# Kernel tuning notes

Measured on AMD Instinct MI355X. Metric: run time of the kernel, lower is better.

The kernel has to match this reference:

```python
import jax, jax.numpy as jnp
import numpy as np

B, T, F_, H1, H2, HEADS = 64, 128, 64, 32, 64, 4
E = H2 * F_  # embed_dim = hidden_dims[-1] * feats = 4096


def conv2d(x, w, b):
    # x: [b,c,H,W], w: [o,c,kh,kw], SAME padding (kernel 3 -> pad 1)
    y = jax.lax.conv_general_dilated(x, w, (1, 1), 'SAME',
                                     dimension_numbers=('NCHW', 'OIHW', 'NCHW'))
    return y + b[None, :, None, None]


def gru_layer(xs, h0, wg, bg, wc, bc):
    # xs: [b,t,c,H,W]; h0: [b,h,H,W]. Standard ConvGRU cell:
    #   r,u = sigmoid(conv([x,h])); cand = tanh(conv([x, r*h]))
    #   h' = (1-u)*h + u*cand
    def step(h, x):
        g = conv2d(jnp.concatenate([x, h], axis=1), wg, bg)
        r, u = jnp.split(jax.nn.sigmoid(g), 2, axis=1)
        cand = jnp.tanh(conv2d(jnp.concatenate([x, r * h], axis=1), wc, bc))
        h_next = (1.0 - u) * h + u * cand
        return h_next, h_next
    hT, ys = jax.lax.scan(step, h0, jnp.swapaxes(xs, 0, 1))
    return jnp.swapaxes(ys, 0, 1), hT  # [b,t,h,H,W], [b,h,H,W]


def mha(q, k, v, w_qkv, b_qkv, w_out, b_out):
    # q: [b,1,E], k/v: [b,t,E]; torch nn.MultiheadAttention (eval, no dropout)
    wq, wk, wv = jnp.split(w_qkv, 3, axis=0)
    bq, bk, bv = jnp.split(b_qkv, 3, axis=0)
    dh = E // HEADS
    def heads(x, w, bb):
        y = x @ w.T + bb
        b_, l_, _ = y.shape
        return y.reshape(b_, l_, HEADS, dh).transpose(0, 2, 1, 3)  # [b,h,l,dh]
    qh, kh, vh = heads(q, wq, bq), heads(k, wk, bk), heads(v, wv, bv)
    scores = jnp.einsum('bhqd,bhkd->bhqk', qh, kh) / jnp.sqrt(jnp.float32(dh))
    attn = jax.nn.softmax(scores, axis=-1)
    ctx = jnp.einsum('bhqk,bhkd->bhqd', attn, vh)
    ctx = ctx.transpose(0, 2, 1, 3).reshape(q.shape[0], q.shape[1], E)
    return ctx @ w_out.T + b_out


def setup_inputs() -> dict:
    key = jax.random.key(0)
    ks = jax.random.split(key, 24)
    s = 0.05
    d = {'x': jax.random.normal(ks[0], (B, T, F_), dtype=jnp.float32)}
    # encoder layer 0: in=1, h=H1; layer 1: in=H1, h=H2
    d['wg_e0'] = jax.random.normal(ks[1], (2 * H1, 1 + H1, 3, 3)) * s
    d['bg_e0'] = jnp.zeros((2 * H1,))
    d['wc_e0'] = jax.random.normal(ks[2], (H1, 1 + H1, 3, 3)) * s
    d['bc_e0'] = jnp.zeros((H1,))
    d['wg_e1'] = jax.random.normal(ks[3], (2 * H2, H1 + H2, 3, 3)) * s
    d['bg_e1'] = jnp.zeros((2 * H2,))
    d['wc_e1'] = jax.random.normal(ks[4], (H2, H1 + H2, 3, 3)) * s
    d['bc_e1'] = jnp.zeros((H2,))
    # decoder: input dim = 2*H2; hidden dims reversed [H2, H1]
    d['wg_d0'] = jax.random.normal(ks[5], (2 * H2, 2 * H2 + H2, 3, 3)) * s
    d['bg_d0'] = jnp.zeros((2 * H2,))
    d['wc_d0'] = jax.random.normal(ks[6], (H2, 2 * H2 + H2, 3, 3)) * s
    d['bc_d0'] = jnp.zeros((H2,))
    d['wg_d1'] = jax.random.normal(ks[7], (2 * H1, H2 + H1, 3, 3)) * s
    d['bg_d1'] = jnp.zeros((2 * H1,))
    d['wc_d1'] = jax.random.normal(ks[8], (H1, H2 + H1, 3, 3)) * s
    d['bc_d1'] = jnp.zeros((H1,))
    d['w_qkv'] = jax.random.normal(ks[9], (3 * E, E)) * (1.0 / np.sqrt(E))
    d['b_qkv'] = jnp.zeros((3 * E,))
    d['w_out'] = jax.random.normal(ks[10], (E, E)) * (1.0 / np.sqrt(E))
    d['b_out'] = jnp.zeros((E,))
    d['w_fin'] = jax.random.normal(ks[11], (1, H1, 1, 1)) * s
    d['b_fin'] = jnp.zeros((1,))
    return d


def reference(x, wg_e0, bg_e0, wc_e0, bc_e0, wg_e1, bg_e1, wc_e1, bc_e1,
              wg_d0, bg_d0, wc_d0, bc_d0, wg_d1, bg_d1, wc_d1, bc_d1,
              w_qkv, b_qkv, w_out, b_out, w_fin, b_fin):
    b, t, f = x.shape
    xr = x.reshape(b, t, 1, f, 1)
    # encoder (2 ConvGRU layers, zero init states)
    y0, h0 = gru_layer(xr, jnp.zeros((b, H1, f, 1), x.dtype), wg_e0, bg_e0, wc_e0, bc_e0)
    y1, h1 = gru_layer(y0, jnp.zeros((b, H2, f, 1), x.dtype), wg_e1, bg_e1, wc_e1, bc_e1)
    # attention bottleneck: query = last hidden, memory = encoder outputs
    query = h1.reshape(b, 1, E)
    memory = y1.reshape(b, t, E)
    context = mha(query, memory, memory, w_qkv, b_qkv, w_out, b_out)  # [b,1,E]
    ctx = context.reshape(b, 1, H2, f, 1)
    dec_in = jnp.concatenate([y1, jnp.broadcast_to(ctx, (b, t, H2, f, 1))], axis=2)
    # decoder init states: encoder last states reversed -> [h1 (H2), h0 (H1)]
    z0, _ = gru_layer(dec_in, h1, wg_d0, bg_d0, wc_d0, bc_d0)
    z1, _ = gru_layer(z0, h0, wg_d1, bg_d1, wc_d1, bc_d1)  # [b,t,H1,f,1]
    # final 1x1 conv applied per timestep == channel contraction
    rec = jnp.einsum('btcfw,oc->btofw', z1, w_fin[:, :, 0, 0]) + b_fin[None, None, :, None, None]
    return rec.reshape(b, t, f)
```

## Files before the change

kernel.cpp:

```cpp
#include <hip/hip_runtime.h>
#include <cstdint>


#define B_  64
#define T_  128
#define TC  16
#define NCH 8

__device__ __forceinline__ float wsum(float v) {
#pragma unroll
  for (int m = 32; m > 0; m >>= 1) v += __shfl_xor(v, m, 64);
  return v;
}
__device__ __forceinline__ float wmaxr(float v) {
#pragma unroll
  for (int m = 32; m > 0; m >>= 1) v = fmaxf(v, __shfl_xor(v, m, 64));
  return v;
}
__device__ __forceinline__ float sigmoidf_(float x) {
  return 1.f / (1.f + __expf(-x));
}
__device__ __forceinline__ float tanhf_(float x) {
  x = fminf(fmaxf(x, -15.f), 15.f);
  float e2 = __expf(2.f * x);
  return (e2 - 1.f) / (e2 + 1.f);
}

struct PackArgs {
  const float* src[16];
  float* dst[16];
  int intot[16];
  int ic0[16];
  int icn[16];
  int oc[16];
};

__global__ __launch_bounds__(256) void pack_all_kernel(PackArgs pa) {
  const int j = blockIdx.y;
  const int icN = pa.icn[j];
  const int total = pa.oc[j] * icN * 3;
  const int i = blockIdx.x * 256 + threadIdx.x;
  if (i >= total) return;
  const int per_oc = icN * 3;
  const int oc = i / per_oc;
  const int rem = i - oc * per_oc;
  const int ic = rem / 3, dk = rem - ic * 3;
  pa.dst[j][i] =
      pa.src[j][((size_t)(oc * pa.intot[j] + pa.ic0[j] + ic) * 3 + dk) * 3 + 1];
}

template <int INC, int OG, int OCC>
__device__ __forceinline__ void conv_x_body(
    float (*sin_)[72], int tid, int b, int tl, int oidx,
    const float* __restrict__ seq, int seqC, size_t sB,
    const float* __restrict__ ctx,
    const float* __restrict__ Wgx, const float* __restrict__ Wcx,
    const float* __restrict__ bg, const float* __restrict__ bc,
    float* __restrict__ out) {
  constexpr int OCT = OG + OCC;
  constexpr int NJ = OG / 32;
  constexpr int NJC = OCC / 32;
  const int ocg = tid >> 3;
  const int f0 = (tid & 7) << 3;

  for (int idx = tid; idx < INC * 72; idx += 256) {
    int ic = idx / 72, ff = idx - ic * 72;
    float v = 0.f;
    if (ff >= 1 && ff <= 64) {
      int fs = ff - 1;
      v = (ic < seqC)
              ? seq[(size_t)b * sB + (size_t)tl * seqC * 64 + ic * 64 + fs]
              : ctx[((size_t)b * (INC - seqC) + (ic - seqC)) * 64 + fs];
    }
    sin_[ic][ff] = v;
  }
  __syncthreads();

  if constexpr (INC >= 4) {
    {
      float acc[NJ][8];
#pragma unroll
      for (int j = 0; j < NJ; ++j) {
        float bb = bg[ocg + 32 * j];
#pragma unroll
        for (int ff = 0; ff < 8; ++ff) acc[j][ff] = bb;
      }
      for (int ic0 = 0; ic0 < INC; ic0 += 4) {
        float hv[4][10];
#pragma unroll
        for (int q = 0; q < 4; ++q) {
          float4 a4 = *(const float4*)&sin_[ic0 + q][f0];
          float4 b4 = *(const float4*)&sin_[ic0 + q][f0 + 4];
          float2 c2 = *(const float2*)&sin_[ic0 + q][f0 + 8];
          hv[q][0] = a4.x; hv[q][1] = a4.y; hv[q][2] = a4.z; hv[q][3] = a4.w;
          hv[q][4] = b4.x; hv[q][5] = b4.y; hv[q][6] = b4.z; hv[q][7] = b4.w;
          hv[q][8] = c2.x; hv[q][9] = c2.y;
        }
#pragma unroll
        for (int j = 0; j < NJ; ++j) {
          const int oc = ocg + 32 * j;
          const float4* w4 = (const float4*)(Wgx + ((size_t)oc * INC + ic0) * 3);
          float4 wa = w4[0], wb = w4[1], wc4 = w4[2];
          const float wt[12] = {wa.x, wa.y, wa.z, wa.w, wb.x, wb.y, wb.z, wb.w,
                                wc4.x, wc4.y, wc4.z, wc4.w};
#pragma unroll
          for (int q = 0; q < 4; ++q) {
            const float w0 = wt[3 * q], w1 = wt[3 * q + 1], w2 = wt[3 * q + 2];
#pragma unroll
            for (int ff = 0; ff < 8; ++ff)
              acc[j][ff] = fmaf(w0, hv[q][ff], fmaf(w1, hv[q][ff + 1], fmaf(w2, hv[q][ff + 2], acc[j][ff])));
          }
        }
      }
#pragma unroll
      for (int j = 0; j < NJ; ++j) {
        float* dst = out + ((size_t)oidx * OCT + ocg + 32 * j) * 64 + f0;
        *(float4*)dst = make_float4(acc[j][0], acc[j][1], acc[j][2], acc[j][3]);
        *(float4*)(dst + 4) = make_float4(acc[j][4], acc[j][5], acc[j][6], acc[j][7]);
      }
    }
    {
      float acc[NJC][8];
#pragma unroll
      for (int j = 0; j < NJC; ++j) {
        float bb = bc[ocg + 32 * j];
#pragma unroll
        for (int ff = 0; ff < 8; ++ff) acc[j][ff] = bb;
      }
      for (int ic0 = 0; ic0 < INC; ic0 += 4) {
        float hv[4][10];
#pragma unroll
        for (int q = 0; q < 4; ++q) {
          float4 a4 = *(const float4*)&sin_[ic0 + q][f0];
          float4 b4 = *(const float4*)&sin_[ic0 + q][f0 + 4];
          float2 c2 = *(const float2*)&sin_[ic0 + q][f0 + 8];
          hv[q][0] = a4.x; hv[q][1] = a4.y; hv[q][2] = a4.z; hv[q][3] = a4.w;
          hv[q][4] = b4.x; hv[q][5] = b4.y; hv[q][6] = b4.z; hv[q][7] = b4.w;
          hv[q][8] = c2.x; hv[q][9] = c2.y;
        }
#pragma unroll
        for (int j = 0; j < NJC; ++j) {
          const int oc = ocg + 32 * j;
          const float4* w4 = (const float4*)(Wcx + ((size_t)oc * INC + ic0) * 3);
          float4 wa = w4[0], wb = w4[1], wc4 = w4[2];
          const float wt[12] = {wa.x, wa.y, wa.z, wa.w, wb.x, wb.y, wb.z, wb.w,
                                wc4.x, wc4.y, wc4.z, wc4.w};
#pragma unroll
          for (int q = 0; q < 4; ++q) {
            const float w0 = wt[3 * q], w1 = wt[3 * q + 1], w2 = wt[3 * q + 2];
#pragma unroll
            for (int ff = 0; ff < 8; ++ff)
              acc[j][ff] = fmaf(w0, hv[q][ff], fmaf(w1, hv[q][ff + 1], fmaf(w2, hv[q][ff + 2], acc[j][ff])));
          }
        }
      }
#pragma unroll
      for (int j = 0; j < NJC; ++j) {
        float* dst = out + ((size_t)oidx * OCT + OG + ocg + 32 * j) * 64 + f0;
        *(float4*)dst = make_float4(acc[j][0], acc[j][1], acc[j][2], acc[j][3]);
        *(float4*)(dst + 4) = make_float4(acc[j][4], acc[j][5], acc[j][6], acc[j][7]);
      }
    }
  } else {
    float hv[10];
    {
      float4 a4 = *(const float4*)&sin_[0][f0];
      float4 b4 = *(const float4*)&sin_[0][f0 + 4];
      float2 c2 = *(const float2*)&sin_[0][f0 + 8];
      hv[0] = a4.x; hv[1] = a4.y; hv[2] = a4.z; hv[3] = a4.w;
      hv[4] = b4.x; hv[5] = b4.y; hv[6] = b4.z; hv[7] = b4.w;
      hv[8] = c2.x; hv[9] = c2.y;
    }
#pragma unroll
    for (int j = 0; j < NJ; ++j) {
      const int oc = ocg + 32 * j;
      const float w0 = Wgx[oc * 3], w1 = Wgx[oc * 3 + 1], w2 = Wgx[oc * 3 + 2];
      float acc[8];
#pragma unroll
      for (int ff = 0; ff < 8; ++ff)
        acc[ff] = fmaf(w0, hv[ff], fmaf(w1, hv[ff + 1], fmaf(w2, hv[ff + 2], bg[oc])));
      float* dst = out + ((size_t)oidx * OCT + oc) * 64 + f0;
      *(float4*)dst = make_float4(acc[0], acc[1], acc[2], acc[3]);
      *(float4*)(dst + 4) = make_float4(acc[4], acc[5], acc[6], acc[7]);
    }
#pragma unroll
    for (int j = 0; j < NJC; ++j) {
      const int oc = ocg + 32 * j;
      const float w0 = Wcx[oc * 3], w1 = Wcx[oc * 3 + 1], w2 = Wcx[oc * 3 + 2];
      float acc[8];
#pragma unroll
      for (int ff = 0; ff < 8; ++ff)
        acc[ff] = fmaf(w0, hv[ff], fmaf(w1, hv[ff + 1], fmaf(w2, hv[ff + 2], bc[oc])));
      float* dst = out + ((size_t)oidx * OCT + OG + oc) * 64 + f0;
      *(float4*)dst = make_float4(acc[0], acc[1], acc[2], acc[3]);
      *(float4*)(dst + 4) = make_float4(acc[4], acc[5], acc[6], acc[7]);
    }
  }
}

template <int INC, int OG, int OCC>
__global__ __launch_bounds__(256) void conv_x_kernel(
    const float* __restrict__ seq, int seqC, size_t sB,
    const float* __restrict__ ctx,
    const float* __restrict__ Wgx, const float* __restrict__ Wcx,
    const float* __restrict__ bg, const float* __restrict__ bc,
    float* __restrict__ out, int tdiv) {
  __shared__ float sin_[INC][72];
  const int b = blockIdx.x / tdiv;
  const int tl = blockIdx.x - b * tdiv;
  conv_x_body<INC, OG, OCC>(sin_, threadIdx.x, b, tl, blockIdx.x, seq, seqC,
                            sB, ctx, Wgx, Wcx, bg, bc, out);
}

__device__ __forceinline__ void final_body(
    int tid, int tile, const float* __restrict__ z1c,
    const float* __restrict__ wfin, const float* __restrict__ bfin,
    float* __restrict__ out, int tOff) {
  const int idx = tile * 256 + tid;
  const int f = idx & 63;
  const int tl = (idx >> 6) & (TC - 1);
  const int b = idx >> 10;
  const float* zp = z1c + ((size_t)b * TC + tl) * 2048 + f;
  float a = bfin[0];
#pragma unroll
  for (int c = 0; c < 32; ++c) a = fmaf(wfin[c], zp[c * 64], a);
  out[(size_t)b * 8192 + (size_t)(tOff + tl) * 64 + f] = a;
}

__global__ __launch_bounds__(256) void final_kernel(
    const float* __restrict__ z1c,
    const float* __restrict__ wfin, const float* __restrict__ bfin,
    float* __restrict__ out, int tOff) {
  final_body(threadIdx.x, blockIdx.x, z1c, wfin, bfin, out, tOff);
}

template <int HC>
__device__ __forceinline__ void gru_body(
    float* smem,
    const float* __restrict__ A, size_t aB,
    const float* __restrict__ Wgh, const float* __restrict__ Wch,
    const float* hinit,
    float* __restrict__ Y, size_t yB, float* hfinal, int b) {
  constexpr int NR = HC / 32;
  constexpr int OG = 2 * HC;
  constexpr int OCT = 3 * HC;
  float(*Hs)[68] = (float(*)[68])smem;
  float(*Rs)[68] = (float(*)[68])(smem + HC * 68);
  const int tid = threadIdx.x;
  const int ocg = tid >> 4;
  const int f0 = (tid & 15) << 2;
  const int im = (f0 == 0) ? 0 : f0 - 1;
  const bool lo = (f0 == 0), hi = (f0 == 60);

  float hreg[NR][4];
#pragma unroll
  for (int r = 0; r < NR; ++r) {
    const int oc = ocg + 32 * r;
    const float4 v = *(const float4*)(hinit + ((size_t)b * HC + oc) * 64 + f0);
    hreg[r][0] = v.x; hreg[r][1] = v.y; hreg[r][2] = v.z; hreg[r][3] = v.w;
    *(float4*)&Hs[oc][f0] = v;
  }
  __syncthreads();
  __builtin_amdgcn_s_setprio(1);

  for (int tl = 0; tl < TC; ++tl) {
    const float* Abt = A + (size_t)b * aB + (size_t)tl * (OCT * 64);
    float accr[NR][4], accu[NR][4], accc[NR][4];
#pragma unroll
    for (int r = 0; r < NR; ++r) {
      const int oc = ocg + 32 * r;
      const float4 vr = *(const float4*)(Abt + (size_t)oc * 64 + f0);
      const float4 vu = *(const float4*)(Abt + (size_t)(HC + oc) * 64 + f0);
      const float4 vc = *(const float4*)(Abt + (size_t)(OG + oc) * 64 + f0);
      accr[r][0] = vr.x; accr[r][1] = vr.y; accr[r][2] = vr.z; accr[r][3] = vr.w;
      accu[r][0] = vu.x; accu[r][1] = vu.y; accu[r][2] = vu.z; accu[r][3] = vu.w;
      accc[r][0] = vc.x; accc[r][1] = vc.y; accc[r][2] = vc.z; accc[r][3] = vc.w;
    }
#pragma unroll 2
    for (int hc0 = 0; hc0 < HC; hc0 += 4) {
      float hv[4][6];
#pragma unroll
      for (int q = 0; q < 4; ++q) {
        const float4 h4 = *(const float4*)&Hs[hc0 + q][f0];
        const float lf = Hs[hc0 + q][im];
        const float rt = Hs[hc0 + q][f0 + 4];
        hv[q][0] = lo ? 0.f : lf;
        hv[q][1] = h4.x; hv[q][2] = h4.y; hv[q][3] = h4.z; hv[q][4] = h4.w;
        hv[q][5] = hi ? 0.f : rt;
      }
#pragma unroll
      for (int r = 0; r < NR; ++r) {
        {
          const float4* w4 = (const float4*)(Wgh + ((size_t)(ocg + 32 * r) * HC + hc0) * 3);
          const float4 wa = w4[0], wb = w4[1], wc4 = w4[2];
          const float wt[12] = {wa.x, wa.y, wa.z, wa.w, wb.x, wb.y, wb.z, wb.w,
                                wc4.x, wc4.y, wc4.z, wc4.w};
#pragma unroll
          for (int q = 0; q < 4; ++q) {
            const float w0 = wt[3 * q], w1 = wt[3 * q + 1], w2 = wt[3 * q + 2];
#pragma unroll
            for (int ff = 0; ff < 4; ++ff)
              accr[r][ff] = fmaf(w0, hv[q][ff], fmaf(w1, hv[q][ff + 1], fmaf(w2, hv[q][ff + 2], accr[r][ff])));
          }
        }
        {
          const float4* w4 = (const float4*)(Wgh + ((size_t)(HC + ocg + 32 * r) * HC + hc0) * 3);
          const float4 wa = w4[0], wb = w4[1], wc4 = w4[2];
          const float wt[12] = {wa.x, wa.y, wa.z, wa.w, wb.x, wb.y, wb.z, wb.w,
                                wc4.x, wc4.y, wc4.z, wc4.w};
#pragma unroll
          for (int q = 0; q < 4; ++q) {
            const float w0 = wt[3 * q], w1 = wt[3 * q + 1], w2 = wt[3 * q + 2];
#pragma unroll
            for (int ff = 0; ff < 4; ++ff)
              accu[r][ff] = fmaf(w0, hv[q][ff], fmaf(w1, hv[q][ff + 1], fmaf(w2, hv[q][ff + 2], accu[r][ff])));
          }
        }
      }
    }
    float uu[NR][4];
#pragma unroll
    for (int r = 0; r < NR; ++r) {
      float4 rh;
#pragma unroll
      for (int ff = 0; ff < 4; ++ff) {
        uu[r][ff] = sigmoidf_(accu[r][ff]);
        (&rh.x)[ff] = sigmoidf_(accr[r][ff]) * hreg[r][ff];
      }
      *(float4*)&Rs[ocg + 32 * r][f0] = rh;
    }
    __syncthreads();
#pragma unroll 2
    for (int hc0 = 0; hc0 < HC; hc0 += 4) {
      float hv[4][6];
#pragma unroll
      for (int q = 0; q < 4; ++q) {
        const float4 h4 = *(const float4*)&Rs[hc0 + q][f0];
        const float lf = Rs[hc0 + q][im];
        const float rt = Rs[hc0 + q][f0 + 4];
        hv[q][0] = lo ? 0.f : lf;
        hv[q][1] = h4.x; hv[q][2] = h4.y; hv[q][3] = h4.z; hv[q][4] = h4.w;
        hv[q][5] = hi ? 0.f : rt;
      }
#pragma unroll
      for (int r = 0; r < NR; ++r) {
        const float4* w4 = (const float4*)(Wch + ((size_t)(ocg + 32 * r) * HC + hc0) * 3);
        const float4 wa = w4[0], wb = w4[1], wc4 = w4[2];
        const float wt[12] = {wa.x, wa.y, wa.z, wa.w, wb.x, wb.y, wb.z, wb.w,
                              wc4.x, wc4.y, wc4.z, wc4.w};
#pragma unroll
        for (int q = 0; q < 4; ++q) {
          const float w0 = wt[3 * q], w1 = wt[3 * q + 1], w2 = wt[3 * q + 2];
#pragma unroll
          for (int ff = 0; ff < 4; ++ff)
            accc[r][ff] = fmaf(w0, hv[q][ff], fmaf(w1, hv[q][ff + 1], fmaf(w2, hv[q][ff + 2], accc[r][ff])));
        }
      }
    }
#pragma unroll
    for (int r = 0; r < NR; ++r) {
      const int oc = ocg + 32 * r;
      float4 yv;
#pragma unroll
      for (int ff = 0; ff < 4; ++ff) {
        const float cd = tanhf_(accc[r][ff]);
        const float hn = fmaf(uu[r][ff], cd - hreg[r][ff], hreg[r][ff]);
        hreg[r][ff] = hn;
        (&yv.x)[ff] = hn;
      }
      *(float4*)(Y + (size_t)b * yB + (size_t)tl * (HC * 64) + (size_t)oc * 64 + f0) = yv;
      *(float4*)&Hs[oc][f0] = yv;
    }
    __syncthreads();
  }
  __builtin_amdgcn_s_setprio(0);
#pragma unroll
  for (int r = 0; r < NR; ++r) {
    const int oc = ocg + 32 * r;
    *(float4*)(hfinal + ((size_t)b * HC + oc) * 64 + f0) =
        make_float4(hreg[r][0], hreg[r][1], hreg[r][2], hreg[r][3]);
  }
}

struct GruArgs {
  const float* A;
  size_t aB;
  const float* Wgh;
  const float* Wch;
  const float* hinit;
  float* Y;
  size_t yB;
  float* hfinal;
};

template <int HC>
__global__ __launch_bounds__(512) void gru_rec_kernel(GruArgs g) {
  __shared__ float smem[2 * HC * 68];
  gru_body<HC>(smem, g.A, g.aB, g.Wgh, g.Wch, g.hinit, g.Y, g.yB, g.hfinal,
               blockIdx.x);
}

__global__ __launch_bounds__(512) void gru_fused_kernel(GruArgs g64, GruArgs g32) {
  __shared__ float smem[2 * 64 * 68];
  if (blockIdx.x < 64) {
    gru_body<64>(smem, g64.A, g64.aB, g64.Wgh, g64.Wch, g64.hinit, g64.Y,
                 g64.yB, g64.hfinal, blockIdx.x);
  } else {
    gru_body<32>(smem, g32.A, g32.aB, g32.Wgh, g32.Wch, g32.hinit, g32.Y,
                 g32.yB, g32.hfinal, blockIdx.x - 64);
  }
}

struct ConvJob {
  int kind;
  int nblk;
  const float* seq;
  int seqC;
  size_t sB;
  const float* ctx;
  const float* w0;
  const float* w1;
  const float* b0;
  const float* b1;
  float* out;
  int tOff;
};

struct MegaArgs {
  GruArgs g64;
  GruArgs g32;
  int ng64, ng32, njobs;
  ConvJob jobs[4];
};

__global__ __launch_bounds__(512) void mega_kernel(MegaArgs ma) {
  __shared__ float smem[18432];
  int bid = blockIdx.x;
  if (bid < ma.ng64) {
    gru_body<64>(smem, ma.g64.A, ma.g64.aB, ma.g64.Wgh, ma.g64.Wch,
                 ma.g64.hinit, ma.g64.Y, ma.g64.yB, ma.g64.hfinal, bid);
    return;
  }
  bid -= ma.ng64;
  if (bid < ma.ng32) {
    gru_body<32>(smem, ma.g32.A, ma.g32.aB, ma.g32.Wgh, ma.g32.Wch,
                 ma.g32.hinit, ma.g32.Y, ma.g32.yB, ma.g32.hfinal, bid);
    return;
  }
  bid -= ma.ng32;
  const int half = threadIdx.x >> 8;
  const int tid = threadIdx.x & 255;
#pragma unroll 1
  for (int j = 0; j < ma.njobs; ++j) {
    if (bid < ma.jobs[j].nblk) {
      const ConvJob cj = ma.jobs[j];
      const int tile = bid * 2 + half;
      const int b = tile >> 4;
      const int tl = tile & (TC - 1);
      if (cj.kind == 2) {
        conv_x_body<128, 128, 64>((float(*)[72])(smem + half * 128 * 72), tid,
                                  b, tl, tile, cj.seq, cj.seqC, cj.sB, cj.ctx,
                                  cj.w0, cj.w1, cj.b0, cj.b1, cj.out);
      } else if (cj.kind == 3) {
        conv_x_body<64, 64, 32>((float(*)[72])(smem + half * 64 * 72), tid,
                                b, tl, tile, cj.seq, cj.seqC, cj.sB, cj.ctx,
                                cj.w0, cj.w1, cj.b0, cj.b1, cj.out);
      } else {
        final_body(tid, tile, cj.seq, cj.w0, cj.b0, cj.out, cj.tOff);
      }
      return;
    }
    bid -= ma.jobs[j].nblk;
  }
}

template <bool WT>
__global__ __launch_bounds__(256) void gemm64_kernel(
    const float* __restrict__ W, int wrs,
    const float* __restrict__ X, int xrs,
    float* __restrict__ O, int ors,
    const float* __restrict__ bias, int K,
    int ebh, size_t hsW, size_t hsX, size_t hsO, size_t hsB) {
  int eb = blockIdx.x;
  if (ebh > 0) {
    int h = blockIdx.x / ebh;
    eb = blockIdx.x - h * ebh;
    W += h * hsW; X += h * hsX; O += h * hsO;
    if (bias) bias += h * hsB;
  }
  const int e0 = eb * 64;
  __shared__ float Xs[64][68];
  __shared__ float Ws[64][68];
  const int tb4 = (threadIdx.x & 15) << 2;
  const int te4 = (threadIdx.x >> 4) << 2;
  float acc[4][4] = {};
  for (int k0 = 0; k0 < K; k0 += 64) {
    {
      const int row = threadIdx.x >> 2;
      const int kq = (threadIdx.x & 3) << 4;
      const float* src = X + (size_t)row * xrs + k0 + kq;
#pragma unroll
      for (int q = 0; q < 4; ++q) {
        float4 v = *(const float4*)(src + (q << 2));
        Xs[kq + (q << 2) + 0][row] = v.x;
        Xs[kq + (q << 2) + 1][row] = v.y;
        Xs[kq + (q << 2) + 2][row] = v.z;
        Xs[kq + (q << 2) + 3][row] = v.w;
      }
    }
    if (!WT) {
      const int row = threadIdx.x >> 2;
      const int kq = (threadIdx.x & 3) << 4;
      const float* src = W + (size_t)(e0 + row) * wrs + k0 + kq;
#pragma unroll
      for (int q = 0; q < 4; ++q) {
        float4 v = *(const float4*)(src + (q << 2));
        Ws[kq + (q << 2) + 0][row] = v.x;
        Ws[kq + (q << 2) + 1][row] = v.y;
        Ws[kq + (q << 2) + 2][row] = v.z;
        Ws[kq + (q << 2) + 3][row] = v.w;
      }
    } else {
      const int row = threadIdx.x >> 2;
      const int eq = (threadIdx.x & 3) << 4;
      const float* src = W + (size_t)(k0 + row) * wrs + e0 + eq;
#pragma unroll
      for (int q = 0; q < 4; ++q)
        *(float4*)&Ws[row][eq + (q << 2)] = *(const float4*)(src + (q << 2));
    }
    __syncthreads();
#pragma unroll 8
    for (int k = 0; k < 64; ++k) {
      float4 xv = *(const float4*)&Xs[k][tb4];
      float4 wv4 = *(const float4*)&Ws[k][te4];
      const float xb[4] = {xv.x, xv.y, xv.z, xv.w};
      const float we[4] = {wv4.x, wv4.y, wv4.z, wv4.w};
#pragma unroll
      for (int i = 0; i < 4; ++i)
#pragma unroll
        for (int j = 0; j < 4; ++j) acc[i][j] = fmaf(xb[i], we[j], acc[i][j]);
    }
    __syncthreads();
  }
#pragma unroll
  for (int i = 0; i < 4; ++i)
#pragma unroll
    for (int j = 0; j < 4; ++j) {
      float v = acc[i][j];
      if (bias) v += bias[e0 + te4 + j];
      O[(size_t)(tb4 + i) * ors + e0 + te4 + j] = v;
    }
}

__global__ __launch_bounds__(256) void attn_scores_kernel(
    const float* __restrict__ qkh, const float* __restrict__ mem,
    float* __restrict__ scores) {
  const int b = blockIdx.x >> 4;
  const int tt = blockIdx.x & 15;
  const int h = threadIdx.x >> 6;
  const int lane = threadIdx.x & 63;
  const float4* qk4 = (const float4*)(qkh + ((size_t)b * 4 + h) * 4096);
#pragma unroll 2
  for (int ti = 0; ti < 8; ++ti) {
    const int t = tt * 8 + ti;
    const float4* m4 = (const float4*)(mem + ((size_t)b * 128 + t) * 4096);
    float s = 0.f;
    for (int e = lane; e < 1024; e += 64) {
      float4 q = qk4[e], m = m4[e];
      s = fmaf(q.x, m.x, fmaf(q.y, m.y, fmaf(q.z, m.z, fmaf(q.w, m.w, s))));
    }
    s = wsum(s);
    if (lane == 0) scores[((size_t)b * 4 + h) * 128 + t] = s;
  }
}

__global__ __launch_bounds__(256) void attn_softmax_kernel(
    const float* __restrict__ scores, const float* __restrict__ qbuf,
    const float* __restrict__ bqkv, float* __restrict__ attnp) {
  const int b = blockIdx.x;
  const int h = threadIdx.x >> 6;
  const int lane = threadIdx.x & 63;
  const float4* q4 = (const float4*)(qbuf + (size_t)b * 4096 + h * 1024);
  const float4* k4 = (const float4*)(bqkv + 4096 + h * 1024);
  float qb = 0.f;
#pragma unroll
  for (int d = lane; d < 256; d += 64) {
    float4 q = q4[d], k = k4[d];
    qb = fmaf(q.x, k.x, fmaf(q.y, k.y, fmaf(q.z, k.z, fmaf(q.w, k.w, qb))));
  }
  qb = wsum(qb);
  const float* sc = scores + ((size_t)b * 4 + h) * 128;
  float s0 = (sc[lane] + qb) * 0.03125f;
  float s1 = (sc[lane + 64] + qb) * 0.03125f;
  float mx = wmaxr(fmaxf(s0, s1));
  float e0v = __expf(s0 - mx), e1v = __expf(s1 - mx);
  float inv = 1.f / wsum(e0v + e1v);
  attnp[((size_t)b * 4 + h) * 128 + lane] = e0v * inv;
  attnp[((size_t)b * 4 + h) * 128 + lane + 64] = e1v * inv;
}

__global__ __launch_bounds__(256) void attn_wsum_kernel(
    const float* __restrict__ attnp, const float* __restrict__ mem,
    float* __restrict__ wmem) {
  const int b = blockIdx.x >> 4;
  const int eb = blockIdx.x & 15;
  const int e = eb * 256 + threadIdx.x;
  __shared__ float ap[4][128];
  for (int i = threadIdx.x; i < 512; i += 256)
    ap[i >> 7][i & 127] = attnp[(size_t)b * 512 + i];
  __syncthreads();
  float a0 = 0, a1 = 0, a2 = 0, a3 = 0;
  const float* mb = mem + (size_t)b * 128 * 4096 + e;
#pragma unroll 4
  for (int t = 0; t < 128; ++t) {
    float m = mb[(size_t)t * 4096];
    a0 = fmaf(ap[0][t], m, a0);
    a1 = fmaf(ap[1][t], m, a1);
    a2 = fmaf(ap[2][t], m, a2);
    a3 = fmaf(ap[3][t], m, a3);
  }
  wmem[((size_t)b * 4 + 0) * 4096 + e] = a0;
  wmem[((size_t)b * 4 + 1) * 4096 + e] = a1;
  wmem[((size_t)b * 4 + 2) * 4096 + e] = a2;
  wmem[((size_t)b * 4 + 3) * 4096 + e] = a3;
}

extern "C" void kernel_launch(void* const* d_in, const int* in_sizes, int n_in,
                              void* d_out, int out_size, void* d_ws, size_t ws_size,
                              hipStream_t stream) {
  (void)in_sizes; (void)n_in; (void)out_size;
  const float* x     = (const float*)d_in[0];
  const float* wg_e0 = (const float*)d_in[1];
  const float* bg_e0 = (const float*)d_in[2];
  const float* wc_e0 = (const float*)d_in[3];
  const float* bc_e0 = (const float*)d_in[4];
  const float* wg_e1 = (const float*)d_in[5];
  const float* bg_e1 = (const float*)d_in[6];
  const float* wc_e1 = (const float*)d_in[7];
  const float* bc_e1 = (const float*)d_in[8];
  const float* wg_d0 = (const float*)d_in[9];
  const float* bg_d0 = (const float*)d_in[10];
  const float* wc_d0 = (const float*)d_in[11];
  const float* bc_d0 = (const float*)d_in[12];
  const float* wg_d1 = (const float*)d_in[13];
  const float* bg_d1 = (const float*)d_in[14];
  const float* wc_d1 = (const float*)d_in[15];
  const float* bc_d1 = (const float*)d_in[16];
  const float* w_qkv = (const float*)d_in[17];
  const float* b_qkv = (const float*)d_in[18];
  const float* w_out = (const float*)d_in[19];
  const float* b_out = (const float*)d_in[20];
  const float* w_fin = (const float*)d_in[21];
  const float* b_fin = (const float*)d_in[22];
  float* out = (float*)d_out;

  float* WS = (float*)d_ws;
  size_t off = 0;
  auto alloc = [&](size_t n) { float* p = WS + off; off += (n + 63) & ~(size_t)63; return p; };
  float* Amp[2] = {alloc((size_t)B_ * TC * 192 * 64), alloc((size_t)B_ * TC * 192 * 64)};
  float* A96full = alloc((size_t)B_ * T_ * 96 * 64);
  float* A96d[2] = {alloc((size_t)B_ * TC * 96 * 64), alloc((size_t)B_ * TC * 96 * 64)};
  float* Y0p[2] = {alloc((size_t)B_ * TC * 32 * 64), alloc((size_t)B_ * TC * 32 * 64)};
  float* Y1   = alloc((size_t)B_ * T_ * 64 * 64);
  float* Z0p[2] = {alloc((size_t)B_ * TC * 64 * 64), alloc((size_t)B_ * TC * 64 * 64)};
  float* Z1p[2] = {alloc((size_t)B_ * TC * 32 * 64), alloc((size_t)B_ * TC * 32 * 64)};
  float* He0p[2] = {alloc((size_t)B_ * 32 * 64), alloc((size_t)B_ * 32 * 64)};
  float* He1p[2] = {alloc((size_t)B_ * 64 * 64), alloc((size_t)B_ * 64 * 64)};
  float* Hd0p[2] = {alloc((size_t)B_ * 64 * 64), alloc((size_t)B_ * 64 * 64)};
  float* Hd1p[2] = {alloc((size_t)B_ * 32 * 64), alloc((size_t)B_ * 32 * 64)};
  float* QBUF = alloc((size_t)B_ * 4096);
  float* QKH  = alloc((size_t)B_ * 4 * 4096);
  float* WMEM = alloc((size_t)B_ * 4 * 4096);
  float* CTXB = alloc((size_t)B_ * 4096);
  float* CTXO = alloc((size_t)B_ * 4096);
  float* SCR  = alloc((size_t)B_ * 4 * 128);
  float* ATTN = alloc((size_t)B_ * 4 * 128);
  float* wgx_e0 = alloc(64 * 1 * 3);    float* wgh_e0 = alloc(64 * 32 * 3);
  float* wcx_e0 = alloc(32 * 1 * 3);    float* wch_e0 = alloc(32 * 32 * 3);
  float* wgx_e1 = alloc(128 * 32 * 3);  float* wgh_e1 = alloc(128 * 64 * 3);
  float* wcx_e1 = alloc(64 * 32 * 3);   float* wch_e1 = alloc(64 * 64 * 3);
  float* wgx_d0 = alloc(128 * 128 * 3); float* wgh_d0 = alloc(128 * 64 * 3);
  float* wcx_d0 = alloc(64 * 128 * 3);  float* wch_d0 = alloc(64 * 64 * 3);
  float* wgx_d1 = alloc(64 * 64 * 3);   float* wgh_d1 = alloc(64 * 32 * 3);
  float* wcx_d1 = alloc(32 * 64 * 3);   float* wch_d1 = alloc(32 * 32 * 3);
  if (ws_size < off * sizeof(float)) return;

  {
    PackArgs pa;
    const float* srcs[16] = {wg_e0, wg_e0, wc_e0, wc_e0, wg_e1, wg_e1, wc_e1, wc_e1,
                             wg_d0, wg_d0, wc_d0, wc_d0, wg_d1, wg_d1, wc_d1, wc_d1};
    float* dsts[16] = {wgx_e0, wgh_e0, wcx_e0, wch_e0, wgx_e1, wgh_e1, wcx_e1, wch_e1,
                       wgx_d0, wgh_d0, wcx_d0, wch_d0, wgx_d1, wgh_d1, wcx_d1, wch_d1};
    int intot[16] = {33, 33, 33, 33, 96, 96, 96, 96, 192, 192, 192, 192, 96, 96, 96, 96};
    int ic0[16]   = {0, 1, 0, 1, 0, 32, 0, 32, 0, 128, 0, 128, 0, 64, 0, 64};
    int icn[16]   = {1, 32, 1, 32, 32, 64, 32, 64, 128, 64, 128, 64, 64, 32, 64, 32};
    int occ[16]   = {64, 64, 32, 32, 128, 128, 64, 64, 128, 128, 64, 64, 64, 64, 32, 32};
    for (int j = 0; j < 16; ++j) {
      pa.src[j] = srcs[j]; pa.dst[j] = dsts[j];
      pa.intot[j] = intot[j]; pa.ic0[j] = ic0[j]; pa.icn[j] = icn[j]; pa.oc[j] = occ[j];
    }
    pack_all_kernel<<<dim3(192, 16), 256, 0, stream>>>(pa);
  }

  hipMemsetAsync(He0p[0], 0, (size_t)B_ * 32 * 64 * 4, stream);
  hipMemsetAsync(He1p[0], 0, (size_t)B_ * 64 * 64 * 4, stream);

  conv_x_kernel<1, 64, 32><<<B_ * T_, 256, 0, stream>>>(
      x, 1, (size_t)T_ * 64, nullptr, wgx_e0, wcx_e0, bg_e0, bc_e0,
      A96full, T_);

  auto g32e = [&](int c) {
    GruArgs g{A96full + (size_t)c * TC * 96 * 64, (size_t)T_ * 96 * 64,
              wgh_e0, wch_e0, He0p[c & 1], Y0p[c & 1], (size_t)TC * 2048,
              He0p[(c + 1) & 1]};
    return g;
  };
  auto conv_e1 = [&](int c) {
    conv_x_kernel<32, 128, 64><<<B_ * TC, 256, 0, stream>>>(
        Y0p[c & 1], 32, (size_t)TC * 2048, nullptr,
        wgx_e1, wcx_e1, bg_e1, bc_e1, Amp[c & 1], TC);
  };

  { GruArgs g = g32e(0); gru_rec_kernel<32><<<64, 512, 0, stream>>>(g); }
  conv_e1(0);
  for (int c = 0; c < NCH; ++c) {
    GruArgs g64 = {Amp[c & 1], (size_t)TC * 192 * 64, wgh_e1, wch_e1,
                   He1p[c & 1], Y1 + (size_t)c * TC * 4096, (size_t)T_ * 4096,
                   He1p[(c + 1) & 1]};
    if (c < NCH - 1) {
      GruArgs g32 = g32e(c + 1);
      gru_fused_kernel<<<128, 512, 0, stream>>>(g64, g32);
      conv_e1(c + 1);
    } else {
      gru_rec_kernel<64><<<64, 512, 0, stream>>>(g64);
    }
  }
  float* He0f = He0p[0];
  float* He1f = He1p[0];

  const float* wq = w_qkv;
  const float* wk = w_qkv + (size_t)4096 * 4096;
  const float* wv = w_qkv + (size_t)8192 * 4096;
  gemm64_kernel<false><<<64, 256, 0, stream>>>(wq, 4096, He1f, 4096, QBUF, 4096,
                                               b_qkv, 4096, 0, 0, 0, 0, 0);
  gemm64_kernel<true><<<256, 256, 0, stream>>>(wk, 4096, QBUF, 4096, QKH, 16384,
                                               nullptr, 1024, 64,
                                               (size_t)1024 * 4096, 1024, 4096, 0);
  attn_scores_kernel<<<B_ * 16, 256, 0, stream>>>(QKH, Y1, SCR);
  attn_softmax_kernel<<<B_, 256, 0, stream>>>(SCR, QBUF, b_qkv, ATTN);
  attn_wsum_kernel<<<B_ * 16, 256, 0, stream>>>(ATTN, Y1, WMEM);
  gemm64_kernel<false><<<64, 256, 0, stream>>>(wv, 4096, WMEM, 16384, CTXB, 4096,
                                               b_qkv + 8192, 4096, 16,
                                               (size_t)1024 * 4096, 4096, 1024, 1024);
  gemm64_kernel<false><<<64, 256, 0, stream>>>(w_out, 4096, CTXB, 4096, CTXO, 4096,
                                               b_out, 4096, 0, 0, 0, 0, 0);

  auto JD0 = [&](int c, float* dst) {
    ConvJob j{}; j.kind = 2; j.nblk = B_ * TC / 2;
    j.seq = Y1 + (size_t)c * TC * 4096; j.seqC = 64; j.sB = (size_t)T_ * 4096;
    j.ctx = CTXO; j.w0 = wgx_d0; j.w1 = wcx_d0; j.b0 = bg_d0; j.b1 = bc_d0;
    j.out = dst; return j;
  };
  auto JD1 = [&](float* z0src, float* dst) {
    ConvJob j{}; j.kind = 3; j.nblk = B_ * TC / 2;
    j.seq = z0src; j.seqC = 64; j.sB = (size_t)TC * 4096;
    j.ctx = nullptr; j.w0 = wgx_d1; j.w1 = wcx_d1; j.b0 = bg_d1; j.b1 = bc_d1;
    j.out = dst; return j;
  };
  auto JFIN = [&](float* z1src, int tOff) {
    ConvJob j{}; j.kind = 4; j.nblk = B_ * TC * 64 / 512;
    j.seq = z1src; j.w0 = w_fin; j.b0 = b_fin; j.out = out; j.tOff = tOff;
    return j;
  };
  auto mega = [&](const GruArgs* a64, const GruArgs* a32, int nj,
                  const ConvJob* js) {
    MegaArgs ma{};
    ma.ng64 = a64 ? 64 : 0; if (a64) ma.g64 = *a64;
    ma.ng32 = a32 ? 64 : 0; if (a32) ma.g32 = *a32;
    ma.njobs = nj;
    int grid = ma.ng64 + ma.ng32;
    for (int i = 0; i < nj; ++i) { ma.jobs[i] = js[i]; grid += js[i].nblk; }
    mega_kernel<<<grid, 512, 0, stream>>>(ma);
  };

  GruArgs gd0[NCH], gd1[NCH];
  for (int c = 0; c < NCH; ++c) {
    gd0[c] = {Amp[c & 1], (size_t)TC * 192 * 64, wgh_d0, wch_d0,
              (c == 0 ? He1f : Hd0p[c & 1]),
              Z0p[c & 1], (size_t)TC * 4096, Hd0p[(c + 1) & 1]};
    gd1[c] = {A96d[c & 1], (size_t)TC * 96 * 64, wgh_d1, wch_d1,
              (c == 0 ? He0f : Hd1p[c & 1]),
              Z1p[c & 1], (size_t)TC * 2048, Hd1p[(c + 1) & 1]};
  }

  conv_x_kernel<128, 128, 64><<<B_ * TC, 256, 0, stream>>>(
      Y1, 64, (size_t)T_ * 4096, CTXO, wgx_d0, wcx_d0, bg_d0, bc_d0,
      Amp[0], TC);
  for (int k = 0; k <= NCH + 1; ++k) {
    const GruArgs* a64 = (k <= NCH - 1) ? &gd0[k] : nullptr;
    const GruArgs* a32 = (k >= 2 && k - 2 <= NCH - 1) ? &gd1[k - 2] : nullptr;
    ConvJob js[4];
    int nj = 0;
    if (k + 1 <= NCH - 1) js[nj++] = JD0(k + 1, Amp[(k + 1) & 1]);
    if (k >= 1 && k - 1 <= NCH - 1)
      js[nj++] = JD1(Z0p[(k - 1) & 1], A96d[(k - 1) & 1]);
    if (k >= 3 && k - 3 <= NCH - 1)
      js[nj++] = JFIN(Z1p[(k - 3) & 1], (k - 3) * TC);
    mega(a64, a32, nj, js);
  }
  final_kernel<<<B_ * TC * 64 / 256, 256, 0, stream>>>(
      Z1p[(NCH - 1) & 1], w_fin, b_fin, out, (NCH - 1) * TC);
}
```

Baseline: 7.282 ms.

## Fuse encoder layer-1 input convolution into layer-0 GRU recurrence blocks

The separate conv_x_kernel launch that computed layer-1 input projections for each chunk is folded into the tail of the layer-0 GRU blocks. Each GRU32 block convolves its own batch's chunk of outputs, two timesteps at a time across the two 256-thread halves. This removes one kernel launch per chunk and puts otherwise idle GRU32 blocks to work. In exchange the convolution runs on only 64 blocks instead of 1024, which may lengthen the critical path of the fused kernel.

```diff
diff --git a/kernel.cpp b/kernel.cpp
--- a/kernel.cpp
+++ b/kernel.cpp
@@ -400,14 +400,47 @@
                blockIdx.x);
 }
 
-__global__ __launch_bounds__(512) void gru_fused_kernel(GruArgs g64, GruArgs g32) {
+struct E1Args {
+  const float* y0;
+  float* dst;
+  const float* wg;
+  const float* wc;
+  const float* bg;
+  const float* bc;
+};
+
+__device__ __forceinline__ void e1_tail(float* smem, int b, const E1Args& e) {
+  __threadfence();
+  const int half = threadIdx.x >> 8;
+  const int tid = threadIdx.x & 255;
+#pragma unroll 1
+  for (int p = 0; p < TC / 2; ++p) {
+    __syncthreads();
+    const int tl = p * 2 + half;
+    conv_x_body<32, 128, 64>((float(*)[72])(smem + half * 32 * 72), tid, b, tl,
+                             b * TC + tl, e.y0, 32, (size_t)TC * 2048, nullptr,
+                             e.wg, e.wc, e.bg, e.bc, e.dst);
+  }
+}
+
+__global__ __launch_bounds__(512) void gru32e_kernel(GruArgs g32, E1Args e1) {
+  __shared__ float smem[2 * 32 * 72];
+  gru_body<32>(smem, g32.A, g32.aB, g32.Wgh, g32.Wch, g32.hinit, g32.Y,
+               g32.yB, g32.hfinal, blockIdx.x);
+  e1_tail(smem, blockIdx.x, e1);
+}
+
+__global__ __launch_bounds__(512) void gru_fused_kernel(GruArgs g64, GruArgs g32,
+                                                        E1Args e1) {
   __shared__ float smem[2 * 64 * 68];
   if (blockIdx.x < 64) {
     gru_body<64>(smem, g64.A, g64.aB, g64.Wgh, g64.Wch, g64.hinit, g64.Y,
                  g64.yB, g64.hfinal, blockIdx.x);
   } else {
+    const int b = blockIdx.x - 64;
     gru_body<32>(smem, g32.A, g32.aB, g32.Wgh, g32.Wch, g32.hinit, g32.Y,
-                 g32.yB, g32.hfinal, blockIdx.x - 64);
+                 g32.yB, g32.hfinal, b);
+    e1_tail(smem, b, e1);
   }
 }
 
@@ -715,22 +748,18 @@
               He0p[(c + 1) & 1]};
     return g;
   };
-  auto conv_e1 = [&](int c) {
-    conv_x_kernel<32, 128, 64><<<B_ * TC, 256, 0, stream>>>(
-        Y0p[c & 1], 32, (size_t)TC * 2048, nullptr,
-        wgx_e1, wcx_e1, bg_e1, bc_e1, Amp[c & 1], TC);
+  auto e1args = [&](int c) {
+    E1Args e{Y0p[c & 1], Amp[c & 1], wgx_e1, wcx_e1, bg_e1, bc_e1};
+    return e;
   };
 
-  { GruArgs g = g32e(0); gru_rec_kernel<32><<<64, 512, 0, stream>>>(g); }
-  conv_e1(0);
+  gru32e_kernel<<<64, 512, 0, stream>>>(g32e(0), e1args(0));
   for (int c = 0; c < NCH; ++c) {
     GruArgs g64 = {Amp[c & 1], (size_t)TC * 192 * 64, wgh_e1, wch_e1,
                    He1p[c & 1], Y1 + (size_t)c * TC * 4096, (size_t)T_ * 4096,
                    He1p[(c + 1) & 1]};
     if (c < NCH - 1) {
-      GruArgs g32 = g32e(c + 1);
-      gru_fused_kernel<<<128, 512, 0, stream>>>(g64, g32);
-      conv_e1(c + 1);
+      gru_fused_kernel<<<128, 512, 0, stream>>>(g64, g32e(c + 1), e1args(c + 1));
     } else {
       gru_rec_kernel<64><<<64, 512, 0, stream>>>(g64);
     }
```

New measurement: 7.469 ms. 2.6% more time.
